# Performance work log

Measured on AMD Instinct MI355X. Metric: run time of the kernel, lower is better.

Reference implementation:

```python
import jax, jax.numpy as jnp
import numpy as np

B, S, H, D = 2, 8192, 16, 64
P = 8            # lsh_num_projs
BS = 256         # block_size
SAMP = 256       # sample_size


def _gray_perm(num_projs):
    # AngularLSH._unit_hamming_distance_array: maps bin ids to Gray-code order
    a = np.array([0, 1], dtype=np.int32)
    for _ in range(num_projs - 1):
        a = np.concatenate([a, np.flip(a) + a.shape[0]])
    return a

_PERM = jnp.asarray(_gray_perm(P))          # (2**P,)
_POW2 = jnp.asarray(2 ** np.arange(P), dtype=jnp.int32)


def setup_inputs() -> dict:
    rng = jax.random.key(0)
    k1, k2, k3, k4, k5 = jax.random.split(rng, 5)
    return {
        "query": jax.random.normal(k1, (B, S, H, D), jnp.float32),
        "key": jax.random.normal(k2, (B, S, H, D), jnp.float32),
        "value": jax.random.normal(k3, (B, S, H, D), jnp.float32),
        "proj_dir": jax.random.normal(k4, (D, P), jnp.float32),
        "sample_idx": jax.random.randint(k5, (B, H, SAMP), 0, S),
    }


def _lsh_hash(x, proj_dir):
    # x: (B,S,H,D) -> Gray-coded bucket ids (B,H,S)
    bits = (jnp.einsum("bshd,dp->bhsp", x, proj_dir) > 0).astype(jnp.int32)
    bins = (bits * _POW2).sum(-1)
    return _PERM[bins]


def _gather_seq(x, idx_bhs):
    # x: (B,S,H,...) gathered along seq by idx (B,H,S)
    idx = jnp.transpose(idx_bhs, (0, 2, 1))  # (B,S,H)
    if x.ndim == 4:
        idx = idx[..., None]
    return jnp.take_along_axis(x, idx, axis=1)


def reference(query, key, value, proj_dir, sample_idx):
    scale = 1.0 / float(np.sqrt(D))
    nb = S // BS

    # --- LSH sort of queries and keys (stable argsort over seq) ---
    q_sort = jnp.argsort(_lsh_hash(query, proj_dir), axis=2)   # (B,H,S)
    k_sort = jnp.argsort(_lsh_hash(key, proj_dir), axis=2)     # (B,H,S)

    q_s = _gather_seq(query, q_sort)   # (B,S,H,D)
    k_s = _gather_seq(key, k_sort)
    v_s = _gather_seq(value, k_sort)

    # --- block-diagonal attention in sorted order ---
    qb = q_s.reshape(B, nb, BS, H, D)
    kb = k_s.reshape(B, nb, BS, H, D)
    vb = v_s.reshape(B, nb, BS, H, D)
    s_blk = jnp.einsum("bnihd,bnjhd->bhnij", qb, kb) * scale   # (B,H,nb,BS,BS)
    lse_blk = jax.nn.logsumexp(s_blk, axis=-1)                 # (B,H,nb,BS)
    a_blk = jnp.einsum("bhnij,bnjhd->bnihd", jax.nn.softmax(s_blk, axis=-1), vb)
    a_blk = a_blk.reshape(B, S, H, D)                          # sorted order
    lse_blk = jnp.transpose(lse_blk, (0, 2, 3, 1)).reshape(B, S, H)

    # un-sort back to original query order
    q_inv = jnp.argsort(q_sort, axis=2)                        # inverse perm (B,H,S)
    a_blk = _gather_seq(a_blk, q_inv)                          # (B,S,H,D)
    lse_blk = _gather_seq(lse_blk, q_inv)                      # (B,S,H)

    # --- residual: uniform sampled-key attention with importance weight ---
    k_r = _gather_seq(key, sample_idx)                         # (B,SAMP,H,D)
    v_r = _gather_seq(value, sample_idx)
    s_r = jnp.einsum("bihd,bjhd->bhij", query, k_r) * scale    # (B,H,S,SAMP)
    lse_r = jax.nn.logsumexp(s_r, axis=-1) + jnp.log(S / SAMP) # (B,H,S)
    a_r = jnp.einsum("bhij,bjhd->bihd", jax.nn.softmax(s_r, axis=-1), v_r)
    lse_r = jnp.transpose(lse_r, (0, 2, 1))                    # (B,S,H)

    # --- combine block + residual estimates via log-sum-exp ---
    lse_t = jnp.logaddexp(lse_blk, lse_r)                      # (B,S,H)
    w_blk = jnp.exp(lse_blk - lse_t)[..., None]
    w_r = jnp.exp(lse_r - lse_t)[..., None]
    attn = a_blk * w_blk + a_r * w_r                           # (B,S,H,D)
    return attn
```

## Files before the change

kernel.cpp:

```cpp
#include <hip/hip_runtime.h>
#include <hip/hip_bf16.h>

#define B 2
#define S 8192
#define H 16
#define D 64
#define NB 32
#define BS 256
#define SAMP 256
#define BH (B*H)
#define BHS (B*H*S)
#define BSHD (B*S*H*D)
#define LOG32 3.4657359027997265f

typedef float f32x4 __attribute__((ext_vector_type(4)));
typedef short bf16x8 __attribute__((ext_vector_type(8)));

__device__ __forceinline__ unsigned int pack2(float a, float b) {
    unsigned int r;
    asm("v_cvt_pk_bf16_f32 %0, %1, %2" : "=v"(r) : "v"(a), "v"(b));
    return r;
}

#define HP 34

__global__ __launch_bounds__(256, 3) void k_hash(const float* __restrict__ q,
                                                 const float* __restrict__ k,
                                                 const float* __restrict__ pd,
                                                 int* __restrict__ hq,
                                                 int* __restrict__ hk,
                                                 unsigned short* __restrict__ kbf) {
    __shared__ float spd4[4 * 520];
    __shared__ unsigned int tile[256 * HP];
    __shared__ int ht[16][16];
    const int t = threadIdx.x;
    for (int i = t; i < 512; i += 256) {
        const float val = pd[i];
        spd4[i] = val; spd4[520 + i] = val;
        spd4[1040 + i] = val; spd4[1560 + i] = val;
    }
    __syncthreads();

    const bool isK = blockIdx.x >= 1024;
    const int  blk = blockIdx.x & 1023;
    const float* src = isK ? k : q;
    int* hdst = isK ? hk : hq;

    const int lane = t & 63;
    const int c    = lane & 3;
    const int rql  = (t >> 6) * 64 + (lane >> 2) * 4;
    const int rowq = blk * 256 + rql;
    const float* sp = spd4 + c * 520;

    float d[4][8];
#pragma unroll
    for (int rr = 0; rr < 4; ++rr)
#pragma unroll
        for (int p = 0; p < 8; ++p) d[rr][p] = 0.f;

#pragma unroll
    for (int j = 0; j < 4; ++j) {
        float4 x[4];
#pragma unroll
        for (int rr = 0; rr < 4; ++rr)
            x[rr] = *(const float4*)(src + ((rowq + rr) << 6) + j * 16 + c * 4);

        if (isK) {
#pragma unroll
            for (int rr = 0; rr < 4; ++rr) {
                uint2 u2;
                u2.x = pack2(x[rr].x, x[rr].y);
                u2.y = pack2(x[rr].z, x[rr].w);
                *(uint2*)&tile[(rql + rr) * HP + j * 8 + c * 2] = u2;
            }
        }
#pragma unroll
        for (int u = 0; u < 4; ++u) {
            const int dim = j * 16 + c * 4 + u;
            float4 s0 = *(const float4*)&sp[dim * 8];
            float4 s1 = *(const float4*)&sp[dim * 8 + 4];
#pragma unroll
            for (int rr = 0; rr < 4; ++rr) {
                const float xv = (u == 0) ? x[rr].x : (u == 1) ? x[rr].y
                               : (u == 2) ? x[rr].z : x[rr].w;
                d[rr][0] += xv * s0.x; d[rr][1] += xv * s0.y;
                d[rr][2] += xv * s0.z; d[rr][3] += xv * s0.w;
                d[rr][4] += xv * s1.x; d[rr][5] += xv * s1.y;
                d[rr][6] += xv * s1.z; d[rr][7] += xv * s1.w;
            }
        }
    }
#pragma unroll
    for (int rr = 0; rr < 4; ++rr)
#pragma unroll
        for (int p = 0; p < 8; ++p) {
            d[rr][p] += __shfl_xor(d[rr][p], 1);
            d[rr][p] += __shfl_xor(d[rr][p], 2);
        }
    int bits[4];
#pragma unroll
    for (int rr = 0; rr < 4; ++rr) {
        int bv = 0;
#pragma unroll
        for (int p = 0; p < 8; ++p) bv |= (d[rr][p] > 0.f) ? (1 << p) : 0;
        bits[rr] = bv;
    }
    const int myb = (c == 0) ? bits[0] : (c == 1) ? bits[1]
                  : (c == 2) ? bits[2] : bits[3];
    const int myrl = rql + c;
    ht[myrl & 15][myrl >> 4] = myb ^ (myb >> 1);
    __syncthreads();

    if (isK) {
        uint4* dst = (uint4*)(kbf + blk * 256 * 64);
#pragma unroll
        for (int it = 0; it < 8; ++it) {
            const int g = it * 256 + t;
            const unsigned int* sl = &tile[(g >> 3) * HP + (g & 7) * 4];
            uint4 val;
            val.x = sl[0]; val.y = sl[1]; val.z = sl[2]; val.w = sl[3];
            dst[g] = val;
        }
    }
    if (t < 64) {
        const int h2 = t >> 2, p2 = t & 3;
        int4 val = *(const int4*)&ht[h2][p2 * 4];
        const int gb = blk >> 9;
        const int s0 = (blk * 16) & (S - 1);
        *(int4*)&hdst[(gb * H + h2) * S + s0 + p2 * 4] = val;
    }
}

#define SORT_NT 64
#define SORT_CH (S / SORT_NT)

__global__ __launch_bounds__(SORT_NT) void k_sort(const int* __restrict__ hq,
                                                  const int* __restrict__ hk,
                                                  int* __restrict__ qs,
                                                  int* __restrict__ ks) {
    __shared__ int hist[SORT_NT * 256];
    __shared__ int base[257];
    const int t  = threadIdx.x;
    const int bh = blockIdx.x & (BH - 1);
    const bool isQ = blockIdx.x < BH;
    const int* hp = (isQ ? hq : hk) + bh * S;
    int*       sp = (isQ ? qs : ks) + bh * S;

    for (int i = 0; i < 256; ++i) hist[t * 256 + i] = 0;
    __syncthreads();
    for (int i = 0; i < SORT_CH; ++i) hist[t * 256 + hp[t * SORT_CH + i]]++;
    __syncthreads();

    for (int bi = 0; bi < 4; ++bi) {
        const int bin = t * 4 + bi;
        int sum = 0;
        for (int tt = 0; tt < SORT_NT; ++tt) sum += hist[tt * 256 + bin];
        base[bin + 1] = sum;
    }
    __syncthreads();
    if (t == 0) {
        base[0] = 0;
        for (int i = 1; i <= 256; ++i) base[i] += base[i - 1];
    }
    __syncthreads();

    for (int bi = 0; bi < 4; ++bi) {
        const int bin = t * 4 + bi;
        int run = base[bin];
        for (int tt = 0; tt < SORT_NT; ++tt) {
            int c = hist[tt * 256 + bin];
            hist[tt * 256 + bin] = run;
            run += c;
        }
    }
    __syncthreads();

    for (int i = 0; i < SORT_CH; ++i) {
        const int s0  = t * SORT_CH + i;
        const int bin = hp[s0];
        sp[hist[t * 256 + bin]++] = s0;
    }
}

#define VP 264
#define PP 40

__global__ __launch_bounds__(512, 2) void k_attn(const float* __restrict__ q,
                                                 const unsigned short* __restrict__ kbf,
                                                 const float* __restrict__ v,
                                                 const int* __restrict__ qs,
                                                 const int* __restrict__ ks,
                                                 const int* __restrict__ sidx,
                                                 float* __restrict__ out) {
    __shared__ __align__(16) unsigned short vT[64 * VP];
    __shared__ __align__(16) unsigned short pL[8 * 32 * PP];

    const int t    = threadIdx.x;
    const int w    = t >> 6;
    const int lane = t & 63;
    const int lg   = lane >> 4;
    const int lr   = lane & 15;
    const int logical = (blockIdx.x & 7) * (BH * NB / 8) + (blockIdx.x >> 3);
    const int blk  = logical & (NB - 1);
    const int bh   = logical >> 5;
    const int h    = bh & (H - 1), b = bh >> 4;
    const int sbase = bh * S + blk * BS;
    unsigned short* pw = pL + w * 32 * PP;

    int qrow[2]; bf16x8 bq[2][2];
#pragma unroll
    for (int qg = 0; qg < 2; ++qg) {
        qrow[qg] = qs[sbase + w * 32 + qg * 16 + lr];
        const float* qp = q + (((b * S + qrow[qg]) * H + h) << 6);
#pragma unroll
        for (int kf = 0; kf < 2; ++kf) {
            float4 x0 = ((const float4*)(qp + kf * 32 + lg * 8))[0];
            float4 x1 = ((const float4*)(qp + kf * 32 + lg * 8))[1];
            union { bf16x8 v8; unsigned int u[4]; } fa;
            fa.u[0] = pack2(x0.x * 0.125f, x0.y * 0.125f);
            fa.u[1] = pack2(x0.z * 0.125f, x0.w * 0.125f);
            fa.u[2] = pack2(x1.x * 0.125f, x1.y * 0.125f);
            fa.u[3] = pack2(x1.z * 0.125f, x1.w * 0.125f);
            bq[qg][kf] = fa.v8;
        }
    }

    float m_run[2] = {-1e30f, -1e30f}, l_run[2] = {0.f, 0.f};
    f32x4 acc[2][4];
#pragma unroll
    for (int qg = 0; qg < 2; ++qg)
#pragma unroll
        for (int dg = 0; dg < 4; ++dg) acc[qg][dg] = (f32x4){0.f, 0.f, 0.f, 0.f};

    for (int pass = 0; pass < 2; ++pass) {
        {
            const int key = t >> 1, d0 = (t & 1) * 32;
            const int krow = pass ? sidx[bh * SAMP + key] : ks[sbase + key];
            const float* vp = v + (((b * S + krow) * H + h) << 6) + d0;
            unsigned int uv[16];
#pragma unroll
            for (int i = 0; i < 8; ++i) {
                float4 y = ((const float4*)vp)[i];
                uv[2 * i]     = pack2(y.x, y.y);
                uv[2 * i + 1] = pack2(y.z, y.w);
            }
            if (pass) __syncthreads();
#pragma unroll
            for (int j = 0; j < 16; ++j) {
                const int d = d0 + 2 * j;
                vT[(d + 0) * VP + key] = (unsigned short)(uv[j]);
                vT[(d + 1) * VP + key] = (unsigned short)(uv[j] >> 16);
            }
        }
        __syncthreads();

        int kidx[4][4];
#pragma unroll
        for (int kt4 = 0; kt4 < 4; ++kt4)
#pragma unroll
            for (int kg = 0; kg < 4; ++kg) {
                const int key = kt4 * 64 + kg * 16 + lr;
                kidx[kt4][kg] = pass ? sidx[bh * SAMP + key] : ks[sbase + key];
            }

        const float bias = pass ? LOG32 : 0.f;
#pragma unroll
        for (int kt4 = 0; kt4 < 4; ++kt4) {
            f32x4 c[2][4];
#pragma unroll
            for (int kf = 0; kf < 2; ++kf) {
                bf16x8 ak[4];
#pragma unroll
                for (int kg = 0; kg < 4; ++kg)
                    ak[kg] = *(const bf16x8*)(kbf + (((b * S + kidx[kt4][kg]) * H + h) << 6)
                                              + kf * 32 + lg * 8);
                __builtin_amdgcn_s_setprio(1);
#pragma unroll
                for (int qg = 0; qg < 2; ++qg)
#pragma unroll
                    for (int kg = 0; kg < 4; ++kg) {
                        f32x4 cin = kf ? c[qg][kg] : (f32x4){0.f, 0.f, 0.f, 0.f};
                        c[qg][kg] = __builtin_amdgcn_mfma_f32_16x16x32_bf16(ak[kg], bq[qg][kf], cin, 0, 0, 0);
                    }
                __builtin_amdgcn_s_setprio(0);
            }
#pragma unroll
            for (int qg = 0; qg < 2; ++qg) {
                float tm = -1e30f;
#pragma unroll
                for (int kg = 0; kg < 4; ++kg)
#pragma unroll
                    for (int r = 0; r < 4; ++r) tm = fmaxf(tm, c[qg][kg][r]);
                tm = fmaxf(tm, __shfl_xor(tm, 16));
                tm = fmaxf(tm, __shfl_xor(tm, 32));
                tm += bias;
                if (!__all(tm <= m_run[qg] + 8.f)) {
                    const float mn  = fmaxf(m_run[qg], tm);
                    const float es  = __expf(m_run[qg] - mn);
                    m_run[qg] = mn;
                    l_run[qg] *= es;
#pragma unroll
                    for (int r = 0; r < 4; ++r) {
                        const float er = __shfl(es, lg * 4 + r);
#pragma unroll
                        for (int dg = 0; dg < 4; ++dg) acc[qg][dg][r] *= er;
                    }
                }
                const float mnb = m_run[qg] - bias;
                float rs = 0.f;
#pragma unroll
                for (int kg = 0; kg < 4; ++kg)
#pragma unroll
                    for (int r = 0; r < 4; ++r) {
                        const float p = __expf(c[qg][kg][r] - mnb);
                        c[qg][kg][r] = p;
                        rs += p;
                    }
                rs += __shfl_xor(rs, 16);
                rs += __shfl_xor(rs, 32);
                l_run[qg] += rs;
            }
#pragma unroll
            for (int hh = 0; hh < 2; ++hh) {
#pragma unroll
                for (int qg = 0; qg < 2; ++qg)
#pragma unroll
                    for (int kg2 = 0; kg2 < 2; ++kg2) {
                        const int kg = hh * 2 + kg2;
                        uint2 u;
                        u.x = pack2(c[qg][kg][0], c[qg][kg][1]);
                        u.y = pack2(c[qg][kg][2], c[qg][kg][3]);
                        *(uint2*)&pw[(qg * 16 + lr) * PP + kg2 * 16 + lg * 4] = u;
                    }
                bf16x8 bv[4];
#pragma unroll
                for (int dg = 0; dg < 4; ++dg)
                    bv[dg] = *(const bf16x8*)&vT[(dg * 16 + lr) * VP + kt4 * 64 + hh * 32 + lg * 8];
                bf16x8 ap[2];
#pragma unroll
                for (int qg = 0; qg < 2; ++qg)
                    ap[qg] = *(const bf16x8*)&pw[(qg * 16 + lr) * PP + lg * 8];
                __builtin_amdgcn_s_setprio(1);
#pragma unroll
                for (int qg = 0; qg < 2; ++qg)
#pragma unroll
                    for (int dg = 0; dg < 4; ++dg)
                        acc[qg][dg] = __builtin_amdgcn_mfma_f32_16x16x32_bf16(ap[qg], bv[dg], acc[qg][dg], 0, 0, 0);
                __builtin_amdgcn_s_setprio(0);
            }
        }
    }

#pragma unroll
    for (int qg = 0; qg < 2; ++qg)
#pragma unroll
        for (int r = 0; r < 4; ++r) {
            const float lq = __shfl(l_run[qg], lg * 4 + r);
            const int   qr = __shfl(qrow[qg], lg * 4 + r);
            const float inv = 1.f / lq;
            const int obase = ((b * S + qr) * H + h) << 6;
#pragma unroll
            for (int dg = 0; dg < 4; ++dg)
                out[obase + dg * 16 + lr] = acc[qg][dg][r] * inv;
        }
}

extern "C" void kernel_launch(void* const* d_in, const int* in_sizes, int n_in,
                              void* d_out, int out_size, void* d_ws, size_t ws_size,
                              hipStream_t stream) {
    const float* q   = (const float*)d_in[0];
    const float* k   = (const float*)d_in[1];
    const float* v   = (const float*)d_in[2];
    const float* pd  = (const float*)d_in[3];
    const int*  sidx = (const int*)d_in[4];
    float* out = (float*)d_out;

    int* hq = (int*)d_ws;
    int* hk = hq + BHS;
    int* qs = hk + BHS;
    int* ks = qs + BHS;
    unsigned short* kbf = (unsigned short*)(ks + BHS);

    k_hash<<<2048, 256, 0, stream>>>(q, k, pd, hq, hk, kbf);
    k_sort<<<2 * BH, SORT_NT, 0, stream>>>(hq, hk, qs, ks);
    k_attn<<<BH * NB, 512, 0, stream>>>(q, kbf, v, qs, ks, sidx, out);
}
```

Measured before the change: 193.1 us.

## Prefetch next K tile fragments, wave-scan sort bins, remap V load threads

Software-pipelines the gathered K fragment loads in the attention loop: the first half of the next 64-key tile's K data is fetched during the current tile's softmax/PV work, instead of all indices and fragments being loaded up front per kf. The sort kernel's serial prefix sum over 256 bins by one thread is replaced with a per-thread 4-bin sum plus a wavefront shuffle scan. The V transpose load mapping is changed so consecutive threads handle consecutive keys. The prefetch adds register pressure, which may hurt occupancy.

```diff
diff --git a/kernel.cpp b/kernel.cpp
--- a/kernel.cpp
+++ b/kernel.cpp
@@ -151,16 +151,25 @@
     for (int i = 0; i < SORT_CH; ++i) hist[t * 256 + hp[t * SORT_CH + i]]++;
     __syncthreads();
 
-    for (int bi = 0; bi < 4; ++bi) {
-        const int bin = t * 4 + bi;
-        int sum = 0;
-        for (int tt = 0; tt < SORT_NT; ++tt) sum += hist[tt * 256 + bin];
-        base[bin + 1] = sum;
-    }
-    __syncthreads();
-    if (t == 0) {
-        base[0] = 0;
-        for (int i = 1; i <= 256; ++i) base[i] += base[i - 1];
+    int v0 = 0, v1 = 0, v2 = 0, v3 = 0;
+    for (int tt = 0; tt < SORT_NT; ++tt) {
+        const int* hr = &hist[tt * 256 + t * 4];
+        v0 += hr[0]; v1 += hr[1]; v2 += hr[2]; v3 += hr[3];
+    }
+    {
+        const int s1 = v0 + v1, s2 = s1 + v2, tot = s2 + v3;
+        int inc = tot;
+#pragma unroll
+        for (int dlt = 1; dlt < 64; dlt <<= 1) {
+            const int n = __shfl_up(inc, dlt);
+            if (t >= dlt) inc += n;
+        }
+        const int ex = inc - tot;
+        base[4 * t + 1] = ex + v0;
+        base[4 * t + 2] = ex + s1;
+        base[4 * t + 3] = ex + s2;
+        base[4 * t + 4] = ex + tot;
+        if (t == 0) base[0] = 0;
     }
     __syncthreads();
 
@@ -234,7 +243,7 @@
 
     for (int pass = 0; pass < 2; ++pass) {
         {
-            const int key = t >> 1, d0 = (t & 1) * 32;
+            const int key = t & 255, d0 = (t >> 8) * 32;
             const int krow = pass ? sidx[bh * SAMP + key] : ks[sbase + key];
             const float* vp = v + (((b * S + krow) * H + h) << 6) + d0;
             unsigned int uv[16];
@@ -254,36 +263,50 @@
         }
         __syncthreads();
 
-        int kidx[4][4];
-#pragma unroll
-        for (int kt4 = 0; kt4 < 4; ++kt4)
-#pragma unroll
-            for (int kg = 0; kg < 4; ++kg) {
-                const int key = kt4 * 64 + kg * 16 + lr;
-                kidx[kt4][kg] = pass ? sidx[bh * SAMP + key] : ks[sbase + key];
-            }
-
         const float bias = pass ? LOG32 : 0.f;
+
+        int krw[4]; bf16x8 akp[4];
+#pragma unroll
+        for (int kg = 0; kg < 4; ++kg) {
+            const int key = kg * 16 + lr;
+            krw[kg] = pass ? sidx[bh * SAMP + key] : ks[sbase + key];
+        }
+#pragma unroll
+        for (int kg = 0; kg < 4; ++kg)
+            akp[kg] = *(const bf16x8*)(kbf + (((b * S + krw[kg]) * H + h) << 6) + lg * 8);
+
 #pragma unroll
         for (int kt4 = 0; kt4 < 4; ++kt4) {
+            bf16x8 ak1[4];
+#pragma unroll
+            for (int kg = 0; kg < 4; ++kg)
+                ak1[kg] = *(const bf16x8*)(kbf + (((b * S + krw[kg]) * H + h) << 6)
+                                           + 32 + lg * 8);
             f32x4 c[2][4];
-#pragma unroll
-            for (int kf = 0; kf < 2; ++kf) {
-                bf16x8 ak[4];
+            __builtin_amdgcn_s_setprio(1);
+#pragma unroll
+            for (int qg = 0; qg < 2; ++qg)
+#pragma unroll
+                for (int kg = 0; kg < 4; ++kg) {
+                    f32x4 z = (f32x4){0.f, 0.f, 0.f, 0.f};
+                    z = __builtin_amdgcn_mfma_f32_16x16x32_bf16(akp[kg], bq[qg][0], z, 0, 0, 0);
+                    c[qg][kg] = __builtin_amdgcn_mfma_f32_16x16x32_bf16(ak1[kg], bq[qg][1], z, 0, 0, 0);
+                }
+            __builtin_amdgcn_s_setprio(0);
+
+            int krwn[4]; bf16x8 akn[4];
+            if (kt4 < 3) {
+#pragma unroll
+                for (int kg = 0; kg < 4; ++kg) {
+                    const int key = (kt4 + 1) * 64 + kg * 16 + lr;
+                    krwn[kg] = pass ? sidx[bh * SAMP + key] : ks[sbase + key];
+                }
 #pragma unroll
                 for (int kg = 0; kg < 4; ++kg)
-                    ak[kg] = *(const bf16x8*)(kbf + (((b * S + kidx[kt4][kg]) * H + h) << 6)
-                                              + kf * 32 + lg * 8);
-                __builtin_amdgcn_s_setprio(1);
-#pragma unroll
-                for (int qg = 0; qg < 2; ++qg)
-#pragma unroll
-                    for (int kg = 0; kg < 4; ++kg) {
-                        f32x4 cin = kf ? c[qg][kg] : (f32x4){0.f, 0.f, 0.f, 0.f};
-                        c[qg][kg] = __builtin_amdgcn_mfma_f32_16x16x32_bf16(ak[kg], bq[qg][kf], cin, 0, 0, 0);
-                    }
-                __builtin_amdgcn_s_setprio(0);
-            }
+                    akn[kg] = *(const bf16x8*)(kbf + (((b * S + krwn[kg]) * H + h) << 6)
+                                               + lg * 8);
+            }
+
 #pragma unroll
             for (int qg = 0; qg < 2; ++qg) {
                 float tm = -1e30f;
@@ -348,6 +371,11 @@
                         acc[qg][dg] = __builtin_amdgcn_mfma_f32_16x16x32_bf16(ap[qg], bv[dg], acc[qg][dg], 0, 0, 0);
                 __builtin_amdgcn_s_setprio(0);
             }
+
+            if (kt4 < 3) {
+#pragma unroll
+                for (int kg = 0; kg < 4; ++kg) { krw[kg] = krwn[kg]; akp[kg] = akn[kg]; }
+            }
         }
     }
 
```

After: 191.2 us. About the same (-1.0%).
